# Kernel tuning notes

Measured on AMD Instinct MI355X. Metric: run time of the kernel, lower is better.

## Reference

```python
import jax, jax.numpy as jnp
import numpy as np

N = 50000      # nodes
E = 800000     # edges (avg degree 16)
IN_DIM, HID, OUT = 128, 128, 64
EPS = 1e-5     # BatchNorm1d eps


def setup_inputs() -> dict:
    key = jax.random.key(0)
    ks = jax.random.split(key, 8)
    x = jax.random.normal(ks[0], (N, IN_DIM), jnp.float32)
    edge_index = jax.random.randint(ks[1], (2, E), 0, N, dtype=jnp.int32)
    def lin(k, i, o):
        return jax.random.normal(k, (i, o), jnp.float32) / np.sqrt(i).astype(np.float32)
    return {
        "x": x,
        "edge_index": edge_index,
        "W1": lin(ks[2], IN_DIM, HID), "b1": jnp.zeros((HID,), jnp.float32),
        "g1": jnp.ones((HID,), jnp.float32), "beta1": jnp.zeros((HID,), jnp.float32),
        "W2": lin(ks[3], HID, HID), "b2": jnp.zeros((HID,), jnp.float32),
        "g2": jnp.ones((HID,), jnp.float32), "beta2": jnp.zeros((HID,), jnp.float32),
        "W3": lin(ks[4], HID, OUT), "b3": jnp.zeros((OUT,), jnp.float32),
    }


def reference(x, edge_index, W1, b1, g1, beta1, W2, b2, g2, beta2, W3, b3):
    # GCNConv normalization: add self-loops, sym norm D^-1/2 (A+I) D^-1/2
    loops = jnp.arange(N, dtype=edge_index.dtype)
    src = jnp.concatenate([edge_index[0], loops])  # message sources
    dst = jnp.concatenate([edge_index[1], loops])  # aggregation targets
    deg = jax.ops.segment_sum(jnp.ones_like(dst, jnp.float32), dst, num_segments=N)
    dis = jnp.where(deg > 0, jax.lax.rsqrt(jnp.maximum(deg, 1.0)), 0.0)
    norm = dis[src] * dis[dst]  # [E+N]

    def conv(h, W, b):
        h = h @ W  # lin before propagation (PyG GCNConv)
        agg = jax.ops.segment_sum(h[src] * norm[:, None], dst, num_segments=N)
        return agg + b  # bias after aggregation

    def bn(h, g, beta):
        # training-mode BatchNorm1d: batch stats over node dim (biased var)
        m = h.mean(axis=0)
        v = h.var(axis=0)
        return g * (h - m) * jax.lax.rsqrt(v + EPS) + beta

    h = jax.nn.relu(bn(conv(x, W1, b1), g1, beta1))   # dropout deterministic (identity)
    h = jax.nn.relu(bn(conv(h, W2, b2), g2, beta2))
    h = conv(h, W3, b3)
    return jax.nn.log_softmax(h, axis=-1)
```

## Files before the change

### kernel.cpp

```cpp
#include <hip/hip_runtime.h>
#include <hip/hip_fp16.h>
#include <math.h>

#define N_NODES 50000
#define N_EDGES 800000
#define BN_EPS 1e-5f
#define CAP 64
#define NPART 256
#define PART 196
#define CHUNK_CAP 48

typedef _Float16 f16x8 __attribute__((ext_vector_type(8)));
typedef _Float16 f16x4 __attribute__((ext_vector_type(4)));
typedef float f32x4 __attribute__((ext_vector_type(4)));

constexpr int GB = (N_NODES + 63) / 64;
constexpr int AB = (N_NODES + 3) / 4;
constexpr int EPB = N_EDGES / NPART;

__global__ __launch_bounds__(256) void setup_partA_k(
    const int* __restrict__ ei, unsigned int* __restrict__ chunk, int* __restrict__ cntT,
    const float* __restrict__ W1, const float* __restrict__ W2, const float* __restrict__ W3,
    __half* __restrict__ Wt1, __half* __restrict__ Wt2, __half* __restrict__ Wt3,
    float* __restrict__ sums) {
    if (blockIdx.x < NPART) {
        __shared__ int cnt[NPART];
        int tid = threadIdx.x, b = blockIdx.x;
        cnt[tid] = 0;
        __syncthreads();
        int lo = b * EPB, hi = lo + EPB;
        for (int e = lo + tid; e < hi; e += 256) {
            int src = ei[e], dst = ei[N_EDGES + e];
            int p = dst / PART;
            int pos = atomicAdd(&cnt[p], 1);
            if (pos < CHUNK_CAP)
                chunk[(unsigned)((b << 8) + p) * CHUNK_CAP + pos] =
                    ((unsigned)dst << 16) | (unsigned)src;
        }
        __syncthreads();
        cntT[tid * NPART + b] = min(cnt[tid], CHUNK_CAP);
    } else {
        int i = (blockIdx.x - NPART) * 256 + threadIdx.x;
        if (i < 512) sums[i] = 0.f;
        if (i < 16384) {
            int k = i >> 7, m = i & 127;
            Wt1[m * 128 + k] = __float2half(W1[i]);
            Wt2[m * 128 + k] = __float2half(W2[i]);
        }
        if (i < 8192) {
            int k = i >> 6, m = i & 63;
            Wt3[m * 128 + k] = __float2half(W3[i]);
        }
    }
}

template <int M, int AF32, int FUSE, int DSCALE, int OUT8>
__device__ __forceinline__ void gemm_body(int bid, int tid,
                                          const void* __restrict__ Av,
                                          const __half* __restrict__ Wt,
                                          const float* __restrict__ sums,
                                          const float* __restrict__ g,
                                          const float* __restrict__ beta,
                                          const int* __restrict__ fil,
                                          void* __restrict__ out) {
    constexpr int NF = M / 32;
    int wid = tid >> 6, lane = tid & 63;

    int rbase = bid * 64 + (wid >> 1) * 32;
    int ncol0 = (wid & 1) * (M / 2);
    int koff = (lane >> 4) * 8;

    int arow[2];
#pragma unroll
    for (int mi = 0; mi < 2; ++mi) {
        int r = rbase + mi * 16 + (lane & 15);
        arow[mi] = (r < N_NODES) ? r : (N_NODES - 1);
    }

    f32x4 acc[2][NF];
#pragma unroll
    for (int mi = 0; mi < 2; ++mi)
#pragma unroll
        for (int ni = 0; ni < NF; ++ni) acc[mi][ni] = (f32x4)(0.f);

#pragma unroll
    for (int k0 = 0; k0 < 128; k0 += 32) {
        float scv[8], shv[8];
        if constexpr (FUSE) {
#pragma unroll
            for (int j = 0; j < 8; ++j) {
                int k = k0 + koff + j;
                float mn = sums[k] * (1.0f / N_NODES);
                float vr = sums[128 + k] * (1.0f / N_NODES) - mn * mn;
                float sc = g[k] * rsqrtf(vr + BN_EPS);
                scv[j] = sc;
                shv[j] = beta[k] - mn * sc;
            }
        }
        f16x8 a[2], b[NF];
#pragma unroll
        for (int mi = 0; mi < 2; ++mi) {
            if constexpr (AF32) {
                const float* Af = (const float*)Av + (size_t)arow[mi] * 128 + k0 + koff;
                float4 p0 = *(const float4*)Af;
                float4 p1 = *(const float4*)(Af + 4);
                a[mi][0] = (_Float16)p0.x; a[mi][1] = (_Float16)p0.y;
                a[mi][2] = (_Float16)p0.z; a[mi][3] = (_Float16)p0.w;
                a[mi][4] = (_Float16)p1.x; a[mi][5] = (_Float16)p1.y;
                a[mi][6] = (_Float16)p1.z; a[mi][7] = (_Float16)p1.w;
            } else {
                f16x8 raw = *(const f16x8*)((const __half*)Av + (size_t)arow[mi] * 128 + k0 + koff);
                if constexpr (FUSE) {
#pragma unroll
                    for (int j = 0; j < 8; ++j)
                        a[mi][j] = (_Float16)fmaxf((float)raw[j] * scv[j] + shv[j], 0.f);
                } else {
                    a[mi] = raw;
                }
            }
        }
#pragma unroll
        for (int ni = 0; ni < NF; ++ni)
            b[ni] = *(const f16x8*)(Wt + (size_t)(ncol0 + ni * 16 + (lane & 15)) * 128 + k0 + koff);
#pragma unroll
        for (int mi = 0; mi < 2; ++mi)
#pragma unroll
            for (int ni = 0; ni < NF; ++ni)
                acc[mi][ni] = __builtin_amdgcn_mfma_f32_16x16x32_f16(b[ni], a[mi], acc[mi][ni], 0, 0, 0);
    }

    int cg = lane >> 4;
#pragma unroll
    for (int mi = 0; mi < 2; ++mi) {
        int grow = rbase + mi * 16 + (lane & 15);
        if (grow < N_NODES) {
            float ds = DSCALE ? rsqrtf((float)fil[grow] + 1.f) : 1.0f;
#pragma unroll
            for (int ni = 0; ni < NF; ++ni) {
                int c = ncol0 + ni * 16 + cg * 4;
                if constexpr (OUT8) {
                    unsigned int w = (unsigned)__builtin_amdgcn_cvt_pk_fp8_f32(
                        acc[mi][ni][0] * ds, acc[mi][ni][1] * ds, 0, false);
                    w = (unsigned)__builtin_amdgcn_cvt_pk_fp8_f32(
                        acc[mi][ni][2] * ds, acc[mi][ni][3] * ds, (int)w, true);
                    *(unsigned int*)((unsigned char*)out + (size_t)grow * M + c) = w;
                } else {
                    f16x4 hv;
#pragma unroll
                    for (int q = 0; q < 4; ++q) hv[q] = (_Float16)(acc[mi][ni][q] * ds);
                    *(f16x4*)((__half*)out + (size_t)grow * M + c) = hv;
                }
            }
        }
    }
}

template <int M, int AF32, int FUSE, int DSCALE, int OUT8>
__global__ __launch_bounds__(256) void mfma_gemm_k(const void* __restrict__ Av,
                                                   const __half* __restrict__ Wt,
                                                   const float* __restrict__ sums,
                                                   const float* __restrict__ g,
                                                   const float* __restrict__ beta,
                                                   const int* __restrict__ fil,
                                                   void* __restrict__ out) {
    gemm_body<M, AF32, FUSE, DSCALE, OUT8>(blockIdx.x, threadIdx.x, Av, Wt, sums, g, beta,
                                           fil, out);
}

__global__ __launch_bounds__(256) void partB_gemm1_k(const float* __restrict__ x,
                                                     const __half* __restrict__ Wt1,
                                                     unsigned char* __restrict__ outh,
                                                     const unsigned int* __restrict__ chunk,
                                                     const int* __restrict__ cntT,
                                                     int* __restrict__ fil,
                                                     unsigned short* __restrict__ bkt) {
    if (blockIdx.x < NPART) {
        __shared__ int cur[PART];
        int p = blockIdx.x, tid = threadIdx.x;
        int dst0 = p * PART;
        for (int i = tid; i < PART; i += 256) cur[i] = 0;
        __syncthreads();
        int n = cntT[p * NPART + tid];
        const unsigned int* cp = chunk + (unsigned)((tid << 8) + p) * CHUNK_CAP;
        int i = 0;
        for (; i + 4 <= n; i += 4) {
            uint4 u4 = *(const uint4*)(cp + i);
#pragma unroll
            for (int j = 0; j < 4; ++j) {
                unsigned u = (j == 0) ? u4.x : (j == 1) ? u4.y : (j == 2) ? u4.z : u4.w;
                int dst = u >> 16, src = u & 0xffff;
                int pos = atomicAdd(&cur[dst - dst0], 1);
                if (pos < CAP) bkt[(size_t)dst * CAP + pos] = (unsigned short)src;
            }
        }
        for (; i < n; ++i) {
            unsigned u = cp[i];
            int dst = u >> 16, src = u & 0xffff;
            int pos = atomicAdd(&cur[dst - dst0], 1);
            if (pos < CAP) bkt[(size_t)dst * CAP + pos] = (unsigned short)src;
        }
        __syncthreads();
        for (int i2 = tid; i2 < PART; i2 += 256) {
            int d = dst0 + i2;
            if (d < N_NODES) fil[d] = cur[i2];
        }
    } else {
        gemm_body<128, 1, 0, 0, 1>(blockIdx.x - NPART, threadIdx.x, x, Wt1, nullptr, nullptr,
                                   nullptr, nullptr, outh);
    }
}

__device__ __forceinline__ void dec8(uint2 u, float* f) {
    f[0] = __builtin_amdgcn_cvt_f32_fp8(u.x, 0);
    f[1] = __builtin_amdgcn_cvt_f32_fp8(u.x, 1);
    f[2] = __builtin_amdgcn_cvt_f32_fp8(u.x, 2);
    f[3] = __builtin_amdgcn_cvt_f32_fp8(u.x, 3);
    f[4] = __builtin_amdgcn_cvt_f32_fp8(u.y, 0);
    f[5] = __builtin_amdgcn_cvt_f32_fp8(u.y, 1);
    f[6] = __builtin_amdgcn_cvt_f32_fp8(u.y, 2);
    f[7] = __builtin_amdgcn_cvt_f32_fp8(u.y, 3);
}

template <int SRCDIS>
__global__ __launch_bounds__(256) void aggh_k(const unsigned char* __restrict__ hs,
                                              const int* __restrict__ fil,
                                              const unsigned short* __restrict__ bkt,
                                              const float* __restrict__ bias,
                                              __half* __restrict__ out) {
    int dst = blockIdx.x * 4 + (threadIdx.x >> 6);
    if (dst >= N_NODES) return;
    int lane = threadIdx.x & 63;
    int qw = lane >> 4, li = lane & 15;
    int cnt = fil[dst];
    int n = min(cnt, CAP);
    float dd = rsqrtf((float)cnt + 1.f);
    const uint2* h2 = (const uint2*)hs;

    float acc[8];
    {
        float sv[8];
        dec8(h2[(size_t)dst * 16 + li], sv);
        float selfw = (qw == 0) ? (SRCDIS ? dd : 1.f) : 0.f;
#pragma unroll
        for (int j = 0; j < 8; ++j) acc[j] = selfw * sv[j];
    }

    const unsigned short* bp = bkt + (size_t)dst * CAP;
    int e = 0;
    for (; e + 16 <= n; e += 16) {
        ushort4 u = *(const ushort4*)(bp + e + qw * 4);
        int s0 = u.x, s1 = u.y, s2 = u.z, s3 = u.w;
        uint2 r0 = h2[(size_t)s0 * 16 + li];
        uint2 r1 = h2[(size_t)s1 * 16 + li];
        uint2 r2 = h2[(size_t)s2 * 16 + li];
        uint2 r3 = h2[(size_t)s3 * 16 + li];
        float w0 = 1.f, w1 = 1.f, w2 = 1.f, w3 = 1.f;
        if constexpr (SRCDIS) {
            w0 = rsqrtf((float)fil[s0] + 1.f);
            w1 = rsqrtf((float)fil[s1] + 1.f);
            w2 = rsqrtf((float)fil[s2] + 1.f);
            w3 = rsqrtf((float)fil[s3] + 1.f);
        }
        float v0[8], v1[8], v2[8], v3[8];
        dec8(r0, v0); dec8(r1, v1); dec8(r2, v2); dec8(r3, v3);
#pragma unroll
        for (int j = 0; j < 8; ++j)
            acc[j] += (w0 * v0[j] + w1 * v1[j]) + (w2 * v2[j] + w3 * v3[j]);
    }
    for (; e + 4 <= n; e += 4) {
        ushort4 u = *(const ushort4*)(bp + e);
        int s = (qw == 0) ? u.x : (qw == 1) ? u.y : (qw == 2) ? u.z : u.w;
        float v[8];
        dec8(h2[(size_t)s * 16 + li], v);
        float w = 1.f;
        if constexpr (SRCDIS) w = rsqrtf((float)fil[s] + 1.f);
#pragma unroll
        for (int j = 0; j < 8; ++j) acc[j] += w * v[j];
    }
    if (e < n) {
        int rem = n - e;
        ushort4 u = *(const ushort4*)(bp + e);
        int s = (qw == 0) ? u.x : (qw == 1) ? u.y : (qw == 2) ? u.z : u.w;
        if (qw < rem) {
            float v[8];
            dec8(h2[(size_t)s * 16 + li], v);
            float w = 1.f;
            if constexpr (SRCDIS) w = rsqrtf((float)fil[s] + 1.f);
#pragma unroll
            for (int j = 0; j < 8; ++j) acc[j] += w * v[j];
        }
    }

#pragma unroll
    for (int j = 0; j < 8; ++j) {
        acc[j] += __shfl_xor(acc[j], 16);
        acc[j] += __shfl_xor(acc[j], 32);
    }

    if (qw == 0) {
        float bv[8];
        *(float4*)bv = *(const float4*)(bias + li * 8);
        *(float4*)(bv + 4) = *(const float4*)(bias + li * 8 + 4);
        f16x8 o;
#pragma unroll
        for (int j = 0; j < 8; ++j) o[j] = (_Float16)(dd * acc[j] + bv[j]);
        *(f16x8*)(out + (size_t)dst * 128 + li * 8) = o;
    }
}

__global__ __launch_bounds__(256) void stats_k(const __half* __restrict__ h,
                                               float* __restrict__ sum, float* __restrict__ sq) {
    __shared__ float ssum[128], ssq[128];
    int tid = threadIdx.x;
    if (tid < 128) { ssum[tid] = 0.f; ssq[tid] = 0.f; }
    __syncthreads();
    float s[8], q[8];
#pragma unroll
    for (int j = 0; j < 8; ++j) { s[j] = 0.f; q[j] = 0.f; }
    const int total = N_NODES * 16;
    int stride = gridDim.x * blockDim.x;
    for (int i = blockIdx.x * blockDim.x + tid; i < total; i += stride) {
        f16x8 v = ((const f16x8*)h)[i];
#pragma unroll
        for (int j = 0; j < 8; ++j) {
            float f = (float)v[j];
            s[j] += f;
            q[j] += f * f;
        }
    }
#pragma unroll
    for (int j = 0; j < 8; ++j) {
        s[j] += __shfl_xor(s[j], 16); s[j] += __shfl_xor(s[j], 32);
        q[j] += __shfl_xor(q[j], 16); q[j] += __shfl_xor(q[j], 32);
    }
    int lane = tid & 63;
    if (lane < 16) {
        int c0 = lane * 8;
#pragma unroll
        for (int j = 0; j < 8; ++j) {
            atomicAdd(&ssum[c0 + j], s[j]);
            atomicAdd(&ssq[c0 + j], q[j]);
        }
    }
    __syncthreads();
    if (tid < 128) {
        atomicAdd(&sum[tid], ssum[tid]);
        atomicAdd(&sq[tid], ssq[tid]);
    }
}

__global__ __launch_bounds__(256) void agg64sm_k(const __half* __restrict__ hs,
                                                 const int* __restrict__ fil,
                                                 const unsigned short* __restrict__ bkt,
                                                 const float* __restrict__ bias,
                                                 float* __restrict__ out) {
    int dst = blockIdx.x * 4 + (threadIdx.x >> 6);
    if (dst >= N_NODES) return;
    int lane = threadIdx.x & 63;
    int g = lane >> 3, l = lane & 7;
    int cnt = fil[dst];
    int n = min(cnt, CAP);
    float dd = rsqrtf((float)cnt + 1.f);
    const f16x8* h8 = (const f16x8*)hs;

    float acc[8];
    {
        f16x8 sv = h8[(size_t)dst * 8 + l];
        float selfw = (g == 0) ? 1.f : 0.f;
#pragma unroll
        for (int j = 0; j < 8; ++j) acc[j] = selfw * (float)sv[j];
    }

    const unsigned short* bp = bkt + (size_t)dst * CAP;
    for (int e0 = 0; e0 < n; e0 += 8) {
        int idx = e0 + g;
        bool act = idx < n;
        int s = act ? bp[idx] : dst;
        f16x8 v = h8[(size_t)s * 8 + l];
        float w = act ? 1.f : 0.f;
#pragma unroll
        for (int j = 0; j < 8; ++j) acc[j] += w * (float)v[j];
    }

#pragma unroll
    for (int j = 0; j < 8; ++j) {
        acc[j] += __shfl_xor(acc[j], 8);
        acc[j] += __shfl_xor(acc[j], 16);
        acc[j] += __shfl_xor(acc[j], 32);
    }

    float bv[8];
    *(float4*)bv = *(const float4*)(bias + l * 8);
    *(float4*)(bv + 4) = *(const float4*)(bias + l * 8 + 4);
    float v[8];
#pragma unroll
    for (int j = 0; j < 8; ++j) v[j] = dd * acc[j] + bv[j];

    float m = v[0];
#pragma unroll
    for (int j = 1; j < 8; ++j) m = fmaxf(m, v[j]);
    m = fmaxf(m, __shfl_xor(m, 1));
    m = fmaxf(m, __shfl_xor(m, 2));
    m = fmaxf(m, __shfl_xor(m, 4));
    float p = 0.f;
#pragma unroll
    for (int j = 0; j < 8; ++j) p += expf(v[j] - m);
    p += __shfl_xor(p, 1);
    p += __shfl_xor(p, 2);
    p += __shfl_xor(p, 4);
    float lse = m + logf(p);

    if (g == 0) {
        float4 o0 = make_float4(v[0] - lse, v[1] - lse, v[2] - lse, v[3] - lse);
        float4 o1 = make_float4(v[4] - lse, v[5] - lse, v[6] - lse, v[7] - lse);
        *(float4*)(out + (size_t)dst * 64 + l * 8) = o0;
        *(float4*)(out + (size_t)dst * 64 + l * 8 + 4) = o1;
    }
}

extern "C" void kernel_launch(void* const* d_in, const int* in_sizes, int n_in,
                              void* d_out, int out_size, void* d_ws, size_t ws_size,
                              hipStream_t stream) {
    const float* x = (const float*)d_in[0];
    const int* ei = (const int*)d_in[1];
    const float* W1 = (const float*)d_in[2];
    const float* b1 = (const float*)d_in[3];
    const float* g1 = (const float*)d_in[4];
    const float* be1 = (const float*)d_in[5];
    const float* W2 = (const float*)d_in[6];
    const float* b2 = (const float*)d_in[7];
    const float* g2 = (const float*)d_in[8];
    const float* be2 = (const float*)d_in[9];
    const float* W3 = (const float*)d_in[10];
    const float* b3 = (const float*)d_in[11];
    float* out = (float*)d_out;

    char* p = (char*)d_ws;
    auto alloc = [&](size_t bytes) {
        void* r = (void*)p;
        p += (bytes + 255) & ~(size_t)255;
        return r;
    };
    int* fil = (int*)alloc(N_NODES * 4);
    unsigned short* bkt = (unsigned short*)alloc((size_t)N_NODES * CAP * 2);
    unsigned int* chunk = (unsigned int*)alloc((size_t)NPART * NPART * CHUNK_CAP * 4);
    int* cntT = (int*)alloc(NPART * NPART * 4);
    float* sums = (float*)alloc(512 * 4);
    __half* Wt1 = (__half*)alloc(128 * 128 * 2);
    __half* Wt2 = (__half*)alloc(128 * 128 * 2);
    __half* Wt3 = (__half*)alloc(64 * 128 * 2);
    unsigned char* buf8 = (unsigned char*)alloc((size_t)N_NODES * 128);
    __half* bufP = (__half*)alloc((size_t)N_NODES * 128 * 2);
    __half* bufQ = (__half*)alloc((size_t)N_NODES * 128 * 2);

    setup_partA_k<<<NPART + 196, 256, 0, stream>>>(ei, chunk, cntT, W1, W2, W3, Wt1, Wt2,
                                                   Wt3, sums);

    partB_gemm1_k<<<NPART + GB, 256, 0, stream>>>(x, Wt1, buf8, chunk, cntT, fil, bkt);
    aggh_k<1><<<AB, 256, 0, stream>>>(buf8, fil, bkt, b1, bufP);
    stats_k<<<1024, 256, 0, stream>>>(bufP, sums, sums + 128);

    mfma_gemm_k<128, 0, 1, 1, 1><<<GB, 256, 0, stream>>>(bufP, Wt2, sums, g1, be1, fil, buf8);
    aggh_k<0><<<AB, 256, 0, stream>>>(buf8, fil, bkt, b2, bufP);
    stats_k<<<1024, 256, 0, stream>>>(bufP, sums + 256, sums + 384);

    mfma_gemm_k<64, 0, 1, 1, 0><<<GB, 256, 0, stream>>>(bufP, Wt3, sums + 256, g2, be2, fil, bufQ);
    agg64sm_k<<<AB, 256, 0, stream>>>(bufQ, fil, bkt, b3, out);
}
```

Measured before the change: 227.7 us.

## Fuse BN statistics into aggregation and split edge partitioning finer

Removes the separate stats kernels that re-read the aggregated activations. Batch-norm sums are instead accumulated inside the aggregation kernel via shared-memory atomics, then spread across 64 global partial slots to reduce atomic contention. A tiny finalize kernel computes scale and shift once, so the GEMM prologue loads precomputed vectors instead of recomputing rsqrt per thread. The edge partition pass also uses 512 blocks with a smaller chunk capacity. This adds per-element shared atomics in the aggregation, and the chunk capacity of 32 per bucket could overflow and drop edges.

New measurement: 276.8 us. 1.22x slower.

```diff
diff --git a/kernel.cpp b/kernel.cpp
--- a/kernel.cpp
+++ b/kernel.cpp
@@ -8,40 +8,41 @@
 #define CAP 64
 #define NPART 256
 #define PART 196
-#define CHUNK_CAP 48
+#define NPA 512
+#define CHUNK_CAP 32
 
 typedef _Float16 f16x8 __attribute__((ext_vector_type(8)));
 typedef _Float16 f16x4 __attribute__((ext_vector_type(4)));
 typedef float f32x4 __attribute__((ext_vector_type(4)));
 
 constexpr int GB = (N_NODES + 63) / 64;
-constexpr int AB = (N_NODES + 3) / 4;
-constexpr int EPB = N_EDGES / NPART;
+constexpr int AB = N_NODES / 4;
+constexpr int EPB = (N_EDGES + NPA - 1) / NPA;
 
 __global__ __launch_bounds__(256) void setup_partA_k(
     const int* __restrict__ ei, unsigned int* __restrict__ chunk, int* __restrict__ cntT,
     const float* __restrict__ W1, const float* __restrict__ W2, const float* __restrict__ W3,
     __half* __restrict__ Wt1, __half* __restrict__ Wt2, __half* __restrict__ Wt3,
-    float* __restrict__ sums) {
-    if (blockIdx.x < NPART) {
+    float* __restrict__ part1, float* __restrict__ part2) {
+    if (blockIdx.x < NPA) {
         __shared__ int cnt[NPART];
         int tid = threadIdx.x, b = blockIdx.x;
         cnt[tid] = 0;
         __syncthreads();
-        int lo = b * EPB, hi = lo + EPB;
+        int lo = b * EPB, hi = min(lo + EPB, N_EDGES);
         for (int e = lo + tid; e < hi; e += 256) {
             int src = ei[e], dst = ei[N_EDGES + e];
             int p = dst / PART;
             int pos = atomicAdd(&cnt[p], 1);
             if (pos < CHUNK_CAP)
-                chunk[(unsigned)((b << 8) + p) * CHUNK_CAP + pos] =
+                chunk[(size_t)((p << 9) | b) * CHUNK_CAP + pos] =
                     ((unsigned)dst << 16) | (unsigned)src;
         }
         __syncthreads();
-        cntT[tid * NPART + b] = min(cnt[tid], CHUNK_CAP);
+        cntT[tid * NPA + b] = min(cnt[tid], CHUNK_CAP);
     } else {
-        int i = (blockIdx.x - NPART) * 256 + threadIdx.x;
-        if (i < 512) sums[i] = 0.f;
+        int i = (blockIdx.x - NPA) * 256 + threadIdx.x;
+        if (i < 16384) { part1[i] = 0.f; part2[i] = 0.f; }
         if (i < 16384) {
             int k = i >> 7, m = i & 127;
             Wt1[m * 128 + k] = __float2half(W1[i]);
@@ -58,9 +59,8 @@
 __device__ __forceinline__ void gemm_body(int bid, int tid,
                                           const void* __restrict__ Av,
                                           const __half* __restrict__ Wt,
-                                          const float* __restrict__ sums,
-                                          const float* __restrict__ g,
-                                          const float* __restrict__ beta,
+                                          const float* __restrict__ scale,
+                                          const float* __restrict__ shift,
                                           const int* __restrict__ fil,
                                           void* __restrict__ out) {
     constexpr int NF = M / 32;
@@ -87,15 +87,10 @@
     for (int k0 = 0; k0 < 128; k0 += 32) {
         float scv[8], shv[8];
         if constexpr (FUSE) {
-#pragma unroll
-            for (int j = 0; j < 8; ++j) {
-                int k = k0 + koff + j;
-                float mn = sums[k] * (1.0f / N_NODES);
-                float vr = sums[128 + k] * (1.0f / N_NODES) - mn * mn;
-                float sc = g[k] * rsqrtf(vr + BN_EPS);
-                scv[j] = sc;
-                shv[j] = beta[k] - mn * sc;
-            }
+            *(float4*)scv = *(const float4*)(scale + k0 + koff);
+            *(float4*)(scv + 4) = *(const float4*)(scale + k0 + koff + 4);
+            *(float4*)shv = *(const float4*)(shift + k0 + koff);
+            *(float4*)(shv + 4) = *(const float4*)(shift + k0 + koff + 4);
         }
         f16x8 a[2], b[NF];
 #pragma unroll
@@ -158,12 +153,11 @@
 template <int M, int AF32, int FUSE, int DSCALE, int OUT8>
 __global__ __launch_bounds__(256) void mfma_gemm_k(const void* __restrict__ Av,
                                                    const __half* __restrict__ Wt,
-                                                   const float* __restrict__ sums,
-                                                   const float* __restrict__ g,
-                                                   const float* __restrict__ beta,
+                                                   const float* __restrict__ scale,
+                                                   const float* __restrict__ shift,
                                                    const int* __restrict__ fil,
                                                    void* __restrict__ out) {
-    gemm_body<M, AF32, FUSE, DSCALE, OUT8>(blockIdx.x, threadIdx.x, Av, Wt, sums, g, beta,
+    gemm_body<M, AF32, FUSE, DSCALE, OUT8>(blockIdx.x, threadIdx.x, Av, Wt, scale, shift,
                                            fil, out);
 }
 
@@ -180,25 +174,29 @@
         int dst0 = p * PART;
         for (int i = tid; i < PART; i += 256) cur[i] = 0;
         __syncthreads();
-        int n = cntT[p * NPART + tid];
-        const unsigned int* cp = chunk + (unsigned)((tid << 8) + p) * CHUNK_CAP;
-        int i = 0;
-        for (; i + 4 <= n; i += 4) {
-            uint4 u4 = *(const uint4*)(cp + i);
-#pragma unroll
-            for (int j = 0; j < 4; ++j) {
-                unsigned u = (j == 0) ? u4.x : (j == 1) ? u4.y : (j == 2) ? u4.z : u4.w;
+#pragma unroll
+        for (int h = 0; h < 2; ++h) {
+            int b = tid + h * 256;
+            int n = cntT[p * NPA + b];
+            const unsigned int* cp = chunk + (size_t)((p << 9) | b) * CHUNK_CAP;
+            int i = 0;
+            for (; i + 4 <= n; i += 4) {
+                uint4 u4 = *(const uint4*)(cp + i);
+#pragma unroll
+                for (int j = 0; j < 4; ++j) {
+                    unsigned u = (j == 0) ? u4.x : (j == 1) ? u4.y : (j == 2) ? u4.z : u4.w;
+                    int dst = u >> 16, src = u & 0xffff;
+                    int pos = atomicAdd(&cur[dst - dst0], 1);
+                    if (pos < CAP) bkt[(size_t)dst * CAP + pos] = (unsigned short)src;
+                }
+            }
+            for (; i < n; ++i) {
+                unsigned u = cp[i];
                 int dst = u >> 16, src = u & 0xffff;
                 int pos = atomicAdd(&cur[dst - dst0], 1);
                 if (pos < CAP) bkt[(size_t)dst * CAP + pos] = (unsigned short)src;
             }
         }
-        for (; i < n; ++i) {
-            unsigned u = cp[i];
-            int dst = u >> 16, src = u & 0xffff;
-            int pos = atomicAdd(&cur[dst - dst0], 1);
-            if (pos < CAP) bkt[(size_t)dst * CAP + pos] = (unsigned short)src;
-        }
         __syncthreads();
         for (int i2 = tid; i2 < PART; i2 += 256) {
             int d = dst0 + i2;
@@ -206,7 +204,7 @@
         }
     } else {
         gemm_body<128, 1, 0, 0, 1>(blockIdx.x - NPART, threadIdx.x, x, Wt1, nullptr, nullptr,
-                                   nullptr, nullptr, outh);
+                                   nullptr, outh);
     }
 }
 
@@ -226,10 +224,15 @@
                                               const int* __restrict__ fil,
                                               const unsigned short* __restrict__ bkt,
                                               const float* __restrict__ bias,
-                                              __half* __restrict__ out) {
-    int dst = blockIdx.x * 4 + (threadIdx.x >> 6);
-    if (dst >= N_NODES) return;
-    int lane = threadIdx.x & 63;
+                                              __half* __restrict__ out,
+                                              float* __restrict__ part) {
+    __shared__ float ssum[128], ssq[128];
+    int tid = threadIdx.x;
+    if (tid < 128) { ssum[tid] = 0.f; ssq[tid] = 0.f; }
+    __syncthreads();
+
+    int dst = blockIdx.x * 4 + (tid >> 6);
+    int lane = tid & 63;
     int qw = lane >> 4, li = lane & 15;
     int cnt = fil[dst];
     int n = min(cnt, CAP);
@@ -301,52 +304,41 @@
         float bv[8];
         *(float4*)bv = *(const float4*)(bias + li * 8);
         *(float4*)(bv + 4) = *(const float4*)(bias + li * 8 + 4);
-        f16x8 o;
-#pragma unroll
-        for (int j = 0; j < 8; ++j) o[j] = (_Float16)(dd * acc[j] + bv[j]);
-        *(f16x8*)(out + (size_t)dst * 128 + li * 8) = o;
-    }
-}
-
-__global__ __launch_bounds__(256) void stats_k(const __half* __restrict__ h,
-                                               float* __restrict__ sum, float* __restrict__ sq) {
-    __shared__ float ssum[128], ssq[128];
-    int tid = threadIdx.x;
-    if (tid < 128) { ssum[tid] = 0.f; ssq[tid] = 0.f; }
+        float o[8];
+        f16x8 oh;
+#pragma unroll
+        for (int j = 0; j < 8; ++j) {
+            o[j] = dd * acc[j] + bv[j];
+            oh[j] = (_Float16)o[j];
+        }
+        *(f16x8*)(out + (size_t)dst * 128 + li * 8) = oh;
+#pragma unroll
+        for (int j = 0; j < 8; ++j) {
+            atomicAdd(&ssum[li * 8 + j], o[j]);
+            atomicAdd(&ssq[li * 8 + j], o[j] * o[j]);
+        }
+    }
     __syncthreads();
-    float s[8], q[8];
-#pragma unroll
-    for (int j = 0; j < 8; ++j) { s[j] = 0.f; q[j] = 0.f; }
-    const int total = N_NODES * 16;
-    int stride = gridDim.x * blockDim.x;
-    for (int i = blockIdx.x * blockDim.x + tid; i < total; i += stride) {
-        f16x8 v = ((const f16x8*)h)[i];
-#pragma unroll
-        for (int j = 0; j < 8; ++j) {
-            float f = (float)v[j];
-            s[j] += f;
-            q[j] += f * f;
-        }
-    }
-#pragma unroll
-    for (int j = 0; j < 8; ++j) {
-        s[j] += __shfl_xor(s[j], 16); s[j] += __shfl_xor(s[j], 32);
-        q[j] += __shfl_xor(q[j], 16); q[j] += __shfl_xor(q[j], 32);
-    }
-    int lane = tid & 63;
-    if (lane < 16) {
-        int c0 = lane * 8;
-#pragma unroll
-        for (int j = 0; j < 8; ++j) {
-            atomicAdd(&ssum[c0 + j], s[j]);
-            atomicAdd(&ssq[c0 + j], q[j]);
-        }
-    }
-    __syncthreads();
-    if (tid < 128) {
-        atomicAdd(&sum[tid], ssum[tid]);
-        atomicAdd(&sq[tid], ssq[tid]);
-    }
+    float* pc = part + ((blockIdx.x & 63) << 8);
+    if (tid < 128) atomicAdd(&pc[tid], ssum[tid]);
+    else atomicAdd(&pc[tid], ssq[tid - 128]);
+}
+
+__global__ void finalize_k(const float* __restrict__ part, const float* __restrict__ g,
+                           const float* __restrict__ beta, float* __restrict__ scale,
+                           float* __restrict__ shift) {
+    int f = threadIdx.x;
+    float s = 0.f, q = 0.f;
+#pragma unroll 8
+    for (int c = 0; c < 64; ++c) {
+        s += part[(c << 8) + f];
+        q += part[(c << 8) + 128 + f];
+    }
+    float mn = s * (1.0f / N_NODES);
+    float vr = q * (1.0f / N_NODES) - mn * mn;
+    float sc = g[f] * rsqrtf(vr + BN_EPS);
+    scale[f] = sc;
+    shift[f] = beta[f] - mn * sc;
 }
 
 __global__ __launch_bounds__(256) void agg64sm_k(const __half* __restrict__ hs,
@@ -443,9 +435,11 @@
     };
     int* fil = (int*)alloc(N_NODES * 4);
     unsigned short* bkt = (unsigned short*)alloc((size_t)N_NODES * CAP * 2);
-    unsigned int* chunk = (unsigned int*)alloc((size_t)NPART * NPART * CHUNK_CAP * 4);
-    int* cntT = (int*)alloc(NPART * NPART * 4);
-    float* sums = (float*)alloc(512 * 4);
+    unsigned int* chunk = (unsigned int*)alloc((size_t)NPART * NPA * CHUNK_CAP * 4);
+    int* cntT = (int*)alloc(NPART * NPA * 4);
+    float* part1 = (float*)alloc(64 * 256 * 4);
+    float* part2 = (float*)alloc(64 * 256 * 4);
+    float* ss = (float*)alloc(512 * 4);
     __half* Wt1 = (__half*)alloc(128 * 128 * 2);
     __half* Wt2 = (__half*)alloc(128 * 128 * 2);
     __half* Wt3 = (__half*)alloc(64 * 128 * 2);
@@ -453,17 +447,17 @@
     __half* bufP = (__half*)alloc((size_t)N_NODES * 128 * 2);
     __half* bufQ = (__half*)alloc((size_t)N_NODES * 128 * 2);
 
-    setup_partA_k<<<NPART + 196, 256, 0, stream>>>(ei, chunk, cntT, W1, W2, W3, Wt1, Wt2,
-                                                   Wt3, sums);
+    setup_partA_k<<<NPA + 64, 256, 0, stream>>>(ei, chunk, cntT, W1, W2, W3, Wt1, Wt2, Wt3,
+                                                part1, part2);
 
     partB_gemm1_k<<<NPART + GB, 256, 0, stream>>>(x, Wt1, buf8, chunk, cntT, fil, bkt);
-    aggh_k<1><<<AB, 256, 0, stream>>>(buf8, fil, bkt, b1, bufP);
-    stats_k<<<1024, 256, 0, stream>>>(bufP, sums, sums + 128);
-
-    mfma_gemm_k<128, 0, 1, 1, 1><<<GB, 256, 0, stream>>>(bufP, Wt2, sums, g1, be1, fil, buf8);
-    aggh_k<0><<<AB, 256, 0, stream>>>(buf8, fil, bkt, b2, bufP);
-    stats_k<<<1024, 256, 0, stream>>>(bufP, sums + 256, sums + 384);
-
-    mfma_gemm_k<64, 0, 1, 1, 0><<<GB, 256, 0, stream>>>(bufP, Wt3, sums + 256, g2, be2, fil, bufQ);
+    aggh_k<1><<<AB, 256, 0, stream>>>(buf8, fil, bkt, b1, bufP, part1);
+    finalize_k<<<1, 128, 0, stream>>>(part1, g1, be1, ss, ss + 128);
+
+    mfma_gemm_k<128, 0, 1, 1, 1><<<GB, 256, 0, stream>>>(bufP, Wt2, ss, ss + 128, fil, buf8);
+    aggh_k<0><<<AB, 256, 0, stream>>>(buf8, fil, bkt, b2, bufP, part2);
+    finalize_k<<<1, 128, 0, stream>>>(part2, g2, be2, ss + 256, ss + 384);
+
+    mfma_gemm_k<64, 0, 1, 1, 0><<<GB, 256, 0, stream>>>(bufP, Wt3, ss + 256, ss + 384, fil, bufQ);
     agg64sm_k<<<AB, 256, 0, stream>>>(bufQ, fil, bkt, b3, out);
 }
```
